# Kernel tuning notes

Measured on AMD Instinct MI355X. Metric: run time of the kernel, lower is better.

## Reference

```python
import jax, jax.numpy as jnp
import numpy as np

N_NODES = 50000
N_EDGES = 800000
D_IN = 128
D_HID = 512
D_OUT = 128


def setup_inputs() -> dict:
    key = jax.random.key(0)
    k1, k2, k3, k4, k5, k6 = jax.random.split(key, 6)
    input_matrix = jax.random.normal(k1, (N_NODES, D_IN), dtype=jnp.float32)
    adjacency_coo_matrix = jax.random.randint(k2, (2, N_EDGES), 0, N_NODES, dtype=jnp.int64)
    # fc net params (torch Linear: y = x @ W.T + b); store W already transposed [D_IN, D_HID]
    lim_fc = 1.0 / np.sqrt(D_IN)
    fc_w = jax.random.uniform(k3, (D_IN, D_HID), dtype=jnp.float32, minval=-lim_fc, maxval=lim_fc)
    fc_b = jax.random.uniform(k4, (D_HID,), dtype=jnp.float32, minval=-lim_fc, maxval=lim_fc)
    # xavier_uniform for [D_IN + D_HID, D_OUT]
    lim_w = np.sqrt(6.0 / (D_IN + D_HID + D_OUT))
    weights_matrix = jax.random.uniform(k5, (D_IN + D_HID, D_OUT), dtype=jnp.float32, minval=-lim_w, maxval=lim_w)
    return {
        "input_matrix": input_matrix,
        "fc_w": fc_w,
        "fc_b": fc_b,
        "weights_matrix": weights_matrix,
        "adjacency_coo_matrix": adjacency_coo_matrix,
    }


def reference(input_matrix, fc_w, fc_b, weights_matrix, adjacency_coo_matrix):
    edge_src, edge_trg = adjacency_coo_matrix[0], adjacency_coo_matrix[1]
    n_nodes = input_matrix.shape[0]
    # gather neighbor features: [E, D_IN]
    neighbors = input_matrix[edge_trg]
    # per-edge MLP + relu: [E, D_HID]
    neighbors_repr = jax.nn.relu(neighbors @ fc_w + fc_b)
    # scatter-max reduce into per-node slots; relu outputs are >= 0, and
    # empty segments map to 0 (matching torch_scatter zero-fill), so clamp at 0
    agg = jax.ops.segment_max(neighbors_repr, edge_src, num_segments=n_nodes)
    agg = jnp.maximum(agg, 0.0)
    concat = jnp.concatenate([input_matrix, agg], axis=1)  # [N, D_IN + D_HID]
    return concat @ weights_matrix  # [N, D_OUT]
```

## Files before the change

kernel.cpp:

```cpp
#include <hip/hip_runtime.h>
#include <hip/hip_bf16.h>

#define N_NODES 50000
#define N_EDGES 800000
#define D_IN 128
#define D_HID 512
#define D_OUT 128
#define CAT_DIM 640
#define CAP 64

typedef __attribute__((ext_vector_type(8))) short short8;
typedef __attribute__((ext_vector_type(4))) float floatx4;

__device__ __forceinline__ unsigned short f2bf(float f) {
    unsigned u = __float_as_uint(f);
    unsigned r = u + 0x7fffu + ((u >> 16) & 1u);
    return (unsigned short)(r >> 16);
}


#define PREP_CASTX_BLOCKS   6250
#define PREP_FCW_BLOCKS      256
#define PREP_W2_BLOCKS       320
#define PREP_DEG_BLOCKS      196
#define PREP_TOTAL_BLOCKS  (PREP_CASTX_BLOCKS + PREP_FCW_BLOCKS + PREP_W2_BLOCKS + PREP_DEG_BLOCKS + 1)

__global__ void prep_kernel(const float* __restrict__ X, const float* __restrict__ fcW,
                            const float* __restrict__ Wm, const int* __restrict__ adj,
                            unsigned short* __restrict__ concat,
                            unsigned short* __restrict__ fcwT,
                            unsigned short* __restrict__ WT,
                            int* __restrict__ deg, int* __restrict__ flag) {
    int b = blockIdx.x;
    int tid = threadIdx.x;
    if (b < PREP_CASTX_BLOCKS) {
        int t = b * 256 + tid;
        int row = t >> 5;
        int cg2 = (t & 31) * 4;
        float4 v = *(const float4*)(X + (size_t)row * D_IN + cg2);
        unsigned short o[4] = { f2bf(v.x), f2bf(v.y), f2bf(v.z), f2bf(v.w) };
        *(unsigned long long*)(concat + (size_t)row * CAT_DIM + cg2) = *(unsigned long long*)o;
        return;
    }
    b -= PREP_CASTX_BLOCKS;
    if (b < PREP_FCW_BLOCKS) {
        int idx = b * 256 + tid;
        int k = idx >> 9;
        int n = idx & (D_HID - 1);
        fcwT[n * D_IN + k] = f2bf(fcW[idx]);
        return;
    }
    b -= PREP_FCW_BLOCKS;
    if (b < PREP_W2_BLOCKS) {
        int idx = b * 256 + tid;
        int k = idx >> 7;
        int n = idx & (D_OUT - 1);
        WT[n * CAT_DIM + k] = f2bf(Wm[idx]);
        return;
    }
    b -= PREP_W2_BLOCKS;
    if (b < PREP_DEG_BLOCKS) {
        int idx = b * 256 + tid;
        if (idx < N_NODES) deg[idx] = 0;
        return;
    }
    if (tid < 64) {
        int v = adj[2 * tid + 1];
        unsigned long long m = __ballot(v != 0);
        if (tid == 0) *flag = (m == 0ULL) ? 2 : 1;
    }
}


__device__ __forceinline__ void hist_edges(const int* __restrict__ adj, int s, int e0,
                                           int* __restrict__ deg, int* __restrict__ edge_list) {
    int src0, src1, trg0, trg1;
    if (s == 2) {
        int4 vs = *(const int4*)(adj + 2 * (size_t)e0);
        int4 vt = *(const int4*)(adj + 2 * ((size_t)N_EDGES + e0));
        src0 = vs.x; src1 = vs.z;
        trg0 = vt.x; trg1 = vt.z;
    } else {
        int2 vs = *(const int2*)(adj + e0);
        int2 vt = *(const int2*)(adj + N_EDGES + e0);
        src0 = vs.x; src1 = vs.y;
        trg0 = vt.x; trg1 = vt.y;
    }
    int p0 = atomicAdd(&deg[src0], 1);
    if (p0 < CAP) edge_list[src0 * CAP + p0] = trg0;
    int p1 = atomicAdd(&deg[src1], 1);
    if (p1 < CAP) edge_list[src1 * CAP + p1] = trg1;
}


#define GPAD 8
#define SM64_BYTES ((64 + 128) * (64 + GPAD) * 2)

template<int BIAS_RELU, int OUT_BF16>
__device__ __forceinline__ void gemm_tile64(char* smem,
    const unsigned short* __restrict__ A, int lda,
    const unsigned short* __restrict__ Bt, int ldb,
    const float* __restrict__ bias, void* __restrict__ Cout, int ldc,
    int M, int K, int bm, int bn)
{
    constexpr int BK = 64;
    typedef unsigned short Row[BK + GPAD];
    Row* As = (Row*)smem;
    Row* Bs = (Row*)(smem + 64 * (BK + GPAD) * 2);
    int tid = threadIdx.x;
    int lane = tid & 63, w = tid >> 6;
    int wm = (w >> 1) * 32, wn = (w & 1) * 64;
    int q = lane >> 4, l16 = lane & 15;
    floatx4 acc[2][4] = {};
    int ra = tid >> 2;
    int ca = (tid & 3) * 8;
    int rb = tid >> 1;
    int cb = (tid & 1) * 8;

    for (int k0 = 0; k0 < K; k0 += BK) {
        {
            int gr = bm + ra;
            const unsigned short* ap = A + (size_t)gr * lda + k0 + ca;
            #pragma unroll
            for (int p = 0; p < 2; ++p) {
                uint4 va = make_uint4(0u, 0u, 0u, 0u);
                if (gr < M) va = *(const uint4*)(ap + p * 32);
                *(uint4*)(&As[ra][ca + p * 32]) = va;
            }
        }
        {
            const unsigned short* bp = Bt + (size_t)(bn + rb) * ldb + k0 + cb;
            #pragma unroll
            for (int p = 0; p < 4; ++p)
                *(uint4*)(&Bs[rb][cb + p * 16]) = *(const uint4*)(bp + p * 16);
        }
        __syncthreads();
        #pragma unroll
        for (int ks = 0; ks < 2; ++ks) {
            short8 af[2], bf[4];
            #pragma unroll
            for (int mi = 0; mi < 2; ++mi)
                af[mi] = *(const short8*)(&As[wm + mi * 16 + l16][ks * 32 + q * 8]);
            #pragma unroll
            for (int ni = 0; ni < 4; ++ni)
                bf[ni] = *(const short8*)(&Bs[wn + ni * 16 + l16][ks * 32 + q * 8]);
            #pragma unroll
            for (int mi = 0; mi < 2; ++mi)
                #pragma unroll
                for (int ni = 0; ni < 4; ++ni)
                    acc[mi][ni] = __builtin_amdgcn_mfma_f32_16x16x32_bf16(af[mi], bf[ni], acc[mi][ni], 0, 0, 0);
        }
        __syncthreads();
    }

    #pragma unroll
    for (int mi = 0; mi < 2; ++mi) {
        #pragma unroll
        for (int ni = 0; ni < 4; ++ni) {
            #pragma unroll
            for (int r = 0; r < 4; ++r) {
                int row = bm + wm + mi * 16 + q * 4 + r;
                int col = bn + wn + ni * 16 + l16;
                if (row < M) {
                    float v = acc[mi][ni][r];
                    if (BIAS_RELU) v = fmaxf(v + bias[col], 0.0f);
                    if (OUT_BF16) ((unsigned short*)Cout)[(size_t)row * ldc + col] = f2bf(v);
                    else          ((float*)Cout)[(size_t)row * ldc + col] = v;
                }
            }
        }
    }
}


#define HIST_VB     1563
#define GEMM1_MT     782
#define GEMM1_TILES (GEMM1_MT * 4)

__global__ __launch_bounds__(256)
void mid_kernel(const int* __restrict__ adj, const int* __restrict__ flag,
                int* __restrict__ deg, int* __restrict__ edge_list,
                const unsigned short* __restrict__ concat,
                const unsigned short* __restrict__ fcwT,
                const float* __restrict__ fcb,
                unsigned short* __restrict__ F) {
    if (blockIdx.x < HIST_VB) {
        int e0 = (blockIdx.x * 256 + threadIdx.x) * 2;
        if (e0 < N_EDGES) hist_edges(adj, flag[0], e0, deg, edge_list);
        return;
    }
    __shared__ char smem[SM64_BYTES];
    int tile = blockIdx.x - HIST_VB;
    gemm_tile64<1, 1>(smem, concat, CAT_DIM, fcwT, D_IN, fcb, F, D_HID,
                      N_NODES, D_IN, (tile >> 2) * 64, (tile & 3) * 128);
}


__device__ __forceinline__ void fmax_bf16x8(float* acc, const uint4& p) {
    const unsigned* a = (const unsigned*)&p;
    #pragma unroll
    for (int j = 0; j < 4; ++j) {
        unsigned u = a[j];
        acc[2 * j]     = fmaxf(acc[2 * j],     __uint_as_float(u << 16));
        acc[2 * j + 1] = fmaxf(acc[2 * j + 1], __uint_as_float(u & 0xffff0000u));
    }
}

__global__ __launch_bounds__(256)
void aggregate_kernel(const unsigned short* __restrict__ F,
                      const int* __restrict__ deg,
                      const int* __restrict__ edge_list,
                      unsigned short* __restrict__ concat) {
    int gw = (blockIdx.x * 256 + threadIdx.x) >> 6;
    if (gw >= N_NODES) return;
    int lane = threadIdx.x & 63;
    int d = deg[gw];
    d = d < CAP ? d : CAP;
    const int* el = edge_list + gw * CAP;
    float acc[8] = {0.f, 0.f, 0.f, 0.f, 0.f, 0.f, 0.f, 0.f};
    int i = 0;
    for (; i + 2 <= d; i += 2) {
        int t0 = el[i], t1 = el[i + 1];
        uint4 p0 = *(const uint4*)(F + (size_t)t0 * D_HID + lane * 8);
        uint4 p1 = *(const uint4*)(F + (size_t)t1 * D_HID + lane * 8);
        fmax_bf16x8(acc, p0);
        fmax_bf16x8(acc, p1);
    }
    if (i < d) {
        uint4 p0 = *(const uint4*)(F + (size_t)el[i] * D_HID + lane * 8);
        fmax_bf16x8(acc, p0);
    }
    unsigned out[4];
    #pragma unroll
    for (int j = 0; j < 4; ++j) {
        unsigned lo = __float_as_uint(acc[2 * j]) >> 16;
        unsigned hi = __float_as_uint(acc[2 * j + 1]) & 0xffff0000u;
        out[j] = lo | hi;
    }
    *(uint4*)(concat + (size_t)gw * CAT_DIM + D_IN + lane * 8) = *(uint4*)out;
}


__global__ __launch_bounds__(256)
void gemm2_kernel(const unsigned short* __restrict__ concat,
                  const unsigned short* __restrict__ WT,
                  float* __restrict__ out) {
    __shared__ char smem[SM64_BYTES];
    gemm_tile64<0, 0>(smem, concat, CAT_DIM, WT, CAT_DIM, nullptr, out, D_OUT,
                      N_NODES, CAT_DIM, blockIdx.x * 64, 0);
}


extern "C" void kernel_launch(void* const* d_in, const int* in_sizes, int n_in,
                              void* d_out, int out_size, void* d_ws, size_t ws_size,
                              hipStream_t stream) {
    const float* X    = (const float*)d_in[0];
    const float* fc_w = (const float*)d_in[1];
    const float* fc_b = (const float*)d_in[2];
    const float* Wm   = (const float*)d_in[3];
    const int*   adj  = (const int*)d_in[4];
    float* outp = (float*)d_out;

    char* ws = (char*)d_ws;
    size_t off = 0;
    auto alloc = [&](size_t bytes) -> void* {
        void* p = ws + off;
        off = (off + bytes + 255) & ~(size_t)255;
        return p;
    };
    unsigned short* concat = (unsigned short*)alloc((size_t)N_NODES * CAT_DIM * 2);
    unsigned short* F      = (unsigned short*)alloc((size_t)N_NODES * D_HID * 2);
    unsigned short* fcwT   = (unsigned short*)alloc((size_t)D_HID * D_IN * 2);
    unsigned short* WT     = (unsigned short*)alloc((size_t)D_OUT * CAT_DIM * 2);
    int* deg       = (int*)alloc((size_t)N_NODES * 4);
    int* edge_list = (int*)alloc((size_t)N_NODES * CAP * 4);
    int* flag      = (int*)alloc(256);

    prep_kernel<<<PREP_TOTAL_BLOCKS, 256, 0, stream>>>(X, fc_w, Wm, adj, concat, fcwT, WT, deg, flag);
    mid_kernel<<<HIST_VB + GEMM1_TILES, 256, 0, stream>>>(adj, flag, deg, edge_list,
                                                          concat, fcwT, fc_b, F);
    aggregate_kernel<<<(N_NODES * 64) / 256, 256, 0, stream>>>(F, deg, edge_list, concat);
    gemm2_kernel<<<GEMM1_MT, 256, 0, stream>>>(concat, WT, outp);
}
```

Measured before the change: 290.9 us.

## Fuse segment-max aggregation with output GEMM via shared-memory concat tile

```diff
diff --git a/kernel.cpp b/kernel.cpp
--- a/kernel.cpp
+++ b/kernel.cpp
@@ -27,7 +27,7 @@
 
 __global__ void prep_kernel(const float* __restrict__ X, const float* __restrict__ fcW,
                             const float* __restrict__ Wm, const int* __restrict__ adj,
-                            unsigned short* __restrict__ concat,
+                            unsigned short* __restrict__ Xb,
                             unsigned short* __restrict__ fcwT,
                             unsigned short* __restrict__ WT,
                             int* __restrict__ deg, int* __restrict__ flag) {
@@ -39,7 +39,7 @@
         int cg2 = (t & 31) * 4;
         float4 v = *(const float4*)(X + (size_t)row * D_IN + cg2);
         unsigned short o[4] = { f2bf(v.x), f2bf(v.y), f2bf(v.z), f2bf(v.w) };
-        *(unsigned long long*)(concat + (size_t)row * CAT_DIM + cg2) = *(unsigned long long*)o;
+        *(unsigned long long*)(Xb + (size_t)row * D_IN + cg2) = *(unsigned long long*)o;
         return;
     }
     b -= PREP_CASTX_BLOCKS;
@@ -180,7 +180,7 @@
 __global__ __launch_bounds__(256)
 void mid_kernel(const int* __restrict__ adj, const int* __restrict__ flag,
                 int* __restrict__ deg, int* __restrict__ edge_list,
-                const unsigned short* __restrict__ concat,
+                const unsigned short* __restrict__ Xb,
                 const unsigned short* __restrict__ fcwT,
                 const float* __restrict__ fcb,
                 unsigned short* __restrict__ F) {
@@ -191,10 +191,14 @@
     }
     __shared__ char smem[SM64_BYTES];
     int tile = blockIdx.x - HIST_VB;
-    gemm_tile64<1, 1>(smem, concat, CAT_DIM, fcwT, D_IN, fcb, F, D_HID,
+    gemm_tile64<1, 1>(smem, Xb, D_IN, fcwT, D_IN, fcb, F, D_HID,
                       N_NODES, D_IN, (tile >> 2) * 64, (tile & 3) * 128);
 }
 
+
+#define AGB_M   32
+#define AGB_LDK (CAT_DIM + 8)
+#define AGG2_BLOCKS 1563
 
 __device__ __forceinline__ void fmax_bf16x8(float* acc, const uint4& p) {
     const unsigned* a = (const unsigned*)&p;
@@ -207,47 +211,85 @@
 }
 
 __global__ __launch_bounds__(256)
-void aggregate_kernel(const unsigned short* __restrict__ F,
+void agg_gemm2_kernel(const unsigned short* __restrict__ F,
                       const int* __restrict__ deg,
                       const int* __restrict__ edge_list,
-                      unsigned short* __restrict__ concat) {
-    int gw = (blockIdx.x * 256 + threadIdx.x) >> 6;
-    if (gw >= N_NODES) return;
-    int lane = threadIdx.x & 63;
-    int d = deg[gw];
-    d = d < CAP ? d : CAP;
-    const int* el = edge_list + gw * CAP;
-    float acc[8] = {0.f, 0.f, 0.f, 0.f, 0.f, 0.f, 0.f, 0.f};
-    int i = 0;
-    for (; i + 2 <= d; i += 2) {
-        int t0 = el[i], t1 = el[i + 1];
-        uint4 p0 = *(const uint4*)(F + (size_t)t0 * D_HID + lane * 8);
-        uint4 p1 = *(const uint4*)(F + (size_t)t1 * D_HID + lane * 8);
-        fmax_bf16x8(acc, p0);
-        fmax_bf16x8(acc, p1);
-    }
-    if (i < d) {
-        uint4 p0 = *(const uint4*)(F + (size_t)el[i] * D_HID + lane * 8);
-        fmax_bf16x8(acc, p0);
-    }
-    unsigned out[4];
+                      const unsigned short* __restrict__ Xb,
+                      const unsigned short* __restrict__ WT,
+                      float* __restrict__ out) {
+    __shared__ unsigned short As[AGB_M][AGB_LDK];
+    int tid = threadIdx.x;
+    int lane = tid & 63, w = tid >> 6;
+    int bm = blockIdx.x * AGB_M;
+
+    {
+        int r = tid >> 3;
+        int c = (tid & 7) * 16;
+        int gr = bm + r;
+        uint4 v0 = make_uint4(0u, 0u, 0u, 0u), v1 = v0;
+        if (gr < N_NODES) {
+            v0 = *(const uint4*)(Xb + (size_t)gr * D_IN + c);
+            v1 = *(const uint4*)(Xb + (size_t)gr * D_IN + c + 8);
+        }
+        *(uint4*)(&As[r][c]) = v0;
+        *(uint4*)(&As[r][c + 8]) = v1;
+    }
+
+    for (int n = 0; n < 8; ++n) {
+        int r = w * 8 + n;
+        int node = bm + r;
+        int d = 0;
+        if (node < N_NODES) { d = deg[node]; d = d < CAP ? d : CAP; }
+        const int* el = edge_list + (size_t)node * CAP;
+        float acc[8] = {0.f, 0.f, 0.f, 0.f, 0.f, 0.f, 0.f, 0.f};
+        int i = 0;
+        for (; i + 4 <= d; i += 4) {
+            int t0 = el[i], t1 = el[i + 1], t2 = el[i + 2], t3 = el[i + 3];
+            uint4 p0 = *(const uint4*)(F + (size_t)t0 * D_HID + lane * 8);
+            uint4 p1 = *(const uint4*)(F + (size_t)t1 * D_HID + lane * 8);
+            uint4 p2 = *(const uint4*)(F + (size_t)t2 * D_HID + lane * 8);
+            uint4 p3 = *(const uint4*)(F + (size_t)t3 * D_HID + lane * 8);
+            fmax_bf16x8(acc, p0);
+            fmax_bf16x8(acc, p1);
+            fmax_bf16x8(acc, p2);
+            fmax_bf16x8(acc, p3);
+        }
+        for (; i < d; ++i) {
+            uint4 p0 = *(const uint4*)(F + (size_t)el[i] * D_HID + lane * 8);
+            fmax_bf16x8(acc, p0);
+        }
+        unsigned o[4];
+        #pragma unroll
+        for (int j = 0; j < 4; ++j) {
+            unsigned lo = __float_as_uint(acc[2 * j]) >> 16;
+            unsigned hi = __float_as_uint(acc[2 * j + 1]) & 0xffff0000u;
+            o[j] = lo | hi;
+        }
+        *(uint4*)(&As[r][D_IN + lane * 8]) = *(uint4*)o;
+    }
+    __syncthreads();
+
+    int wm = (w >> 1) * 16, wn = (w & 1) * 64;
+    int q = lane >> 4, l16 = lane & 15;
+    floatx4 acc[4] = {};
+    #pragma unroll 4
+    for (int step = 0; step < CAT_DIM / 32; ++step) {
+        short8 af = *(const short8*)(&As[wm + l16][step * 32 + q * 8]);
+        #pragma unroll
+        for (int ni = 0; ni < 4; ++ni) {
+            short8 bf = *(const short8*)(WT + (size_t)(wn + ni * 16 + l16) * CAT_DIM + step * 32 + q * 8);
+            acc[ni] = __builtin_amdgcn_mfma_f32_16x16x32_bf16(af, bf, acc[ni], 0, 0, 0);
+        }
+    }
     #pragma unroll
-    for (int j = 0; j < 4; ++j) {
-        unsigned lo = __float_as_uint(acc[2 * j]) >> 16;
-        unsigned hi = __float_as_uint(acc[2 * j + 1]) & 0xffff0000u;
-        out[j] = lo | hi;
-    }
-    *(uint4*)(concat + (size_t)gw * CAT_DIM + D_IN + lane * 8) = *(uint4*)out;
-}
-
-
-__global__ __launch_bounds__(256)
-void gemm2_kernel(const unsigned short* __restrict__ concat,
-                  const unsigned short* __restrict__ WT,
-                  float* __restrict__ out) {
-    __shared__ char smem[SM64_BYTES];
-    gemm_tile64<0, 0>(smem, concat, CAT_DIM, WT, CAT_DIM, nullptr, out, D_OUT,
-                      N_NODES, CAT_DIM, blockIdx.x * 64, 0);
+    for (int ni = 0; ni < 4; ++ni) {
+        #pragma unroll
+        for (int r = 0; r < 4; ++r) {
+            int row = bm + wm + q * 4 + r;
+            int col = wn + ni * 16 + l16;
+            if (row < N_NODES) out[(size_t)row * D_OUT + col] = acc[ni][r];
+        }
+    }
 }
 
 
@@ -268,7 +310,7 @@
         off = (off + bytes + 255) & ~(size_t)255;
         return p;
     };
-    unsigned short* concat = (unsigned short*)alloc((size_t)N_NODES * CAT_DIM * 2);
+    unsigned short* Xb     = (unsigned short*)alloc((size_t)N_NODES * D_IN * 2);
     unsigned short* F      = (unsigned short*)alloc((size_t)N_NODES * D_HID * 2);
     unsigned short* fcwT   = (unsigned short*)alloc((size_t)D_HID * D_IN * 2);
     unsigned short* WT     = (unsigned short*)alloc((size_t)D_OUT * CAT_DIM * 2);
@@ -276,9 +318,8 @@
     int* edge_list = (int*)alloc((size_t)N_NODES * CAP * 4);
     int* flag      = (int*)alloc(256);
 
-    prep_kernel<<<PREP_TOTAL_BLOCKS, 256, 0, stream>>>(X, fc_w, Wm, adj, concat, fcwT, WT, deg, flag);
+    prep_kernel<<<PREP_TOTAL_BLOCKS, 256, 0, stream>>>(X, fc_w, Wm, adj, Xb, fcwT, WT, deg, flag);
     mid_kernel<<<HIST_VB + GEMM1_TILES, 256, 0, stream>>>(adj, flag, deg, edge_list,
-                                                          concat, fcwT, fc_b, F);
-    aggregate_kernel<<<(N_NODES * 64) / 256, 256, 0, stream>>>(F, deg, edge_list, concat);
-    gemm2_kernel<<<GEMM1_MT, 256, 0, stream>>>(concat, WT, outp);
-}
+                                                          Xb, fcwT, fc_b, F);
+    agg_gemm2_kernel<<<AGG2_BLOCKS, 256, 0, stream>>>(F, deg, edge_list, Xb, WT, outp);
+}
```

Result: slower. 337.8 us (+16.1%).
